# Kernel optimization log

Hardware: AMD Instinct MI355X
Metric: run time of the kernel (lower is better)

The kernel has to match this reference:

```python
import jax, jax.numpy as jnp
import numpy as np

EPS = 1e-8
MIN_VAL = -1e7  # min_val for masked_max padding


def _cos(v1, v2, axis=-1):
    # torch.F.cosine_similarity: dot / (max(||v1||,eps) * max(||v2||,eps))
    n1 = jnp.maximum(jnp.linalg.norm(v1, axis=axis), EPS)
    n2 = jnp.maximum(jnp.linalg.norm(v2, axis=axis), EPS)
    return jnp.sum(v1 * v2, axis=axis) / (n1 * n2)


def _mpm(v1, v2, w):
    # v1: (B,S,H), v2: (B,S,H) or (B,1,H), w: (P,H)
    mv_one = _cos(v1, v2)[..., None]                 # (B,S,1)
    v1w = w[None, None] * v1[:, :, None, :]          # (B,S,P,H)
    v2w = w[None, None] * v2[:, :, None, :]          # (B,S or 1,P,H)
    mv_many = _cos(v1w, v2w)                          # (B,S,P)
    return mv_one, mv_many


def _mpm_pairwise(v1, v2, w):
    # v1: (B,S1,H), v2: (B,S2,H), w: (P,H) -> (B,S1,S2,P)
    v1w = w[None, :, None, :] * v1[:, None]          # (B,P,S1,H)
    v2w = w[None, :, None, :] * v2[:, None]          # (B,P,S2,H)
    n1 = jnp.linalg.norm(v1w, axis=3)[..., None]     # (B,P,S1,1)
    n2 = jnp.linalg.norm(v2w, axis=3)[..., None]     # (B,P,S2,1)
    mul = jnp.einsum('bpih,bpjh->bpij', v1w, v2w)    # (B,P,S1,S2)
    norm = jnp.maximum(n1 * jnp.swapaxes(n2, 2, 3), EPS)
    return jnp.transpose(mul / norm, (0, 2, 3, 1))


def _masked_max(v, m, axis, keepdims=False):
    return jnp.max(v + (1.0 - m) * MIN_VAL, axis=axis, keepdims=keepdims)


def _masked_mean(v, m, axis, keepdims=False):
    s = jnp.sum(v, axis=axis, keepdims=keepdims)
    c = jnp.sum(m, axis=axis, keepdims=keepdims)
    return s / jnp.maximum(c, EPS)


def _bimpm(context_p, mask_p, context_h, mask_h, w_full, w_maxpool, w_att, w_maxatt):
    mp = mask_p.astype(context_p.dtype)              # (B,S1)
    mh = mask_h.astype(context_h.dtype)              # (B,S2)
    len_p = jnp.sum(mask_p, axis=1)
    len_h = jnp.sum(mask_h, axis=1)
    cp = context_p * mp[..., None]
    ch = context_h * mh[..., None]

    # pairwise cosine similarity (B,S1,S2)
    cos = _cos(cp[:, :, None, :], ch[:, None, :, :])
    cos_max_p = _masked_max(cos, mh[:, None, :], 2, True)
    cos_mean_p = _masked_mean(cos, mh[:, None, :], 2, True)
    cosT = jnp.swapaxes(cos, 1, 2)
    cos_max_h = _masked_max(cosT, mp[:, None, :], 2, True)
    cos_mean_h = _masked_mean(cosT, mp[:, None, :], 2, True)
    mv_p = [cos_max_p, cos_mean_p]
    mv_h = [cos_max_h, cos_mean_h]

    # full match (is_forward=True -> use last valid token)
    B, _, H = cp.shape
    idx_p = jnp.maximum(len_p - 1, 0)[:, None, None]
    idx_h = jnp.maximum(len_h - 1, 0)[:, None, None]
    last_p = jnp.take_along_axis(cp, jnp.broadcast_to(idx_p, (B, 1, H)), axis=1)
    last_h = jnp.take_along_axis(ch, jnp.broadcast_to(idx_h, (B, 1, H)), axis=1)
    o, m = _mpm(cp, last_h, w_full); mv_p += [o, m]
    o, m = _mpm(ch, last_p, w_full); mv_h += [o, m]

    # maxpool match over pairwise multi-perspective cosines (B,S1,S2,P)
    pw = _mpm_pairwise(cp, ch, w_maxpool)
    mv_p += [_masked_max(pw, mh[:, None, :, None], 2),
             _masked_mean(pw, mh[:, None, :, None], 2)]
    pwT = jnp.transpose(pw, (0, 2, 1, 3))
    mv_h += [_masked_max(pwT, mp[:, None, :, None], 2),
             _masked_mean(pwT, mp[:, None, :, None], 2)]

    # attentive match (mean-weighted by cosine attention)
    att = cos
    att_mean_h = jnp.einsum('bij,bjh->bih', att, ch) / jnp.maximum(
        jnp.sum(att, axis=2, keepdims=True), EPS)        # (B,S1,H)
    att_mean_p = jnp.einsum('bij,bih->bjh', att, cp) / jnp.maximum(
        jnp.swapaxes(jnp.sum(att, axis=1, keepdims=True), 1, 2), EPS)  # (B,S2,H)
    o, m = _mpm(cp, att_mean_h, w_att); mv_p += [o, m]
    o, m = _mpm(ch, att_mean_p, w_att); mv_h += [o, m]

    # max attentive match
    att_h_full = ch[:, None, :, :] * att[..., None]      # (B,S1,S2,H)
    att_max_h = _masked_max(att_h_full, mh[:, None, :, None], 2)  # (B,S1,H)
    att_p_full = cp[:, :, None, :] * att[..., None]      # (B,S1,S2,H)
    att_max_p = _masked_max(att_p_full, mp[:, :, None, None], 1)  # (B,S2,H)
    o, m = _mpm(cp, att_max_h, w_maxatt); mv_p += [o, m]
    o, m = _mpm(ch, att_max_p, w_maxatt); mv_h += [o, m]

    # (2, B, S, output_dim=105)
    return jnp.stack([jnp.concatenate(mv_p, axis=-1),
                      jnp.concatenate(mv_h, axis=-1)], axis=0)


def setup_inputs() -> dict:
    B, S1, S2, H, P = 8, 256, 256, 100, 20
    key = jax.random.key(0)
    ks = jax.random.split(key, 8)
    context_p = jax.random.normal(ks[0], (B, S1, H), jnp.float32)
    context_h = jax.random.normal(ks[1], (B, S2, H), jnp.float32)
    len_p = jax.random.randint(ks[2], (B,), S1 // 2, S1 + 1)
    len_h = jax.random.randint(ks[3], (B,), S2 // 2, S2 + 1)
    mask_p = (jnp.arange(S1)[None, :] < len_p[:, None]).astype(jnp.int32)
    mask_h = (jnp.arange(S2)[None, :] < len_h[:, None]).astype(jnp.int32)
    # four matching weights (share_weight_between_directions=True), torch.rand -> U[0,1)
    w_full = jax.random.uniform(ks[4], (P, H), jnp.float32)
    w_maxpool = jax.random.uniform(ks[5], (P, H), jnp.float32)
    w_att = jax.random.uniform(ks[6], (P, H), jnp.float32)
    w_maxatt = jax.random.uniform(ks[7], (P, H), jnp.float32)
    return {"context_p": context_p, "mask_p": mask_p, "context_h": context_h,
            "mask_h": mask_h, "w_full": w_full, "w_maxpool": w_maxpool,
            "w_att": w_att, "w_maxatt": w_maxatt}


def reference(context_p, mask_p, context_h, mask_h, w_full, w_maxpool, w_att, w_maxatt):
    return _bimpm(context_p, mask_p, context_h, mask_h, w_full, w_maxpool, w_att, w_maxatt)
```

## Files before the change

kernel.cpp:

```cpp
#include <hip/hip_runtime.h>

#define Bq 8
#define Sq 256
#define Hq 100
#define Pq 20
#define PPq 21
#define Fq 105
#define EPSq 1e-8f
#define NEGB -1e30f
#define IMG (128 * 136)

typedef short bf16x8 __attribute__((ext_vector_type(8)));
typedef float f32x4 __attribute__((ext_vector_type(4)));

__device__ __forceinline__ unsigned fkey(float f) {
    unsigned b = __float_as_uint(f);
    return (b & 0x80000000u) ? ~b : (b | 0x80000000u);
}
__device__ __forceinline__ float funkey(unsigned k) {
    return __uint_as_float((k & 0x80000000u) ? (k ^ 0x80000000u) : ~k);
}
__device__ __forceinline__ unsigned short bf16rn(float f) {
    unsigned u = __float_as_uint(f);
    unsigned r = u + 0x7FFFu + ((u >> 16) & 1u);
    return (unsigned short)(r >> 16);
}
__device__ __forceinline__ unsigned mulpack(unsigned pair, float w0, float w1) {
    float f0 = __uint_as_float(pair << 16);
    float f1 = __uint_as_float(pair & 0xFFFF0000u);
    f0 *= w0; f1 *= w1;
    return ((unsigned)bf16rn(f0)) | (((unsigned)bf16rn(f1)) << 16);
}

__global__ __launch_bounds__(256) void k_prep(
    const float* __restrict__ ctx_p, const int* __restrict__ mask_p,
    const float* __restrict__ ctx_h, const int* __restrict__ mask_h,
    const float* __restrict__ w_mp,
    float* __restrict__ vm, float* __restrict__ vmT,
    float* __restrict__ mf, float* __restrict__ wn,
    unsigned short* __restrict__ a16,
    float* __restrict__ lens, int* __restrict__ lasts,
    unsigned* __restrict__ statinit) {
    __shared__ float tileT[Hq * 65];
    __shared__ float w2T[Hq * 20];
    __shared__ float redp[PPq * 4 * 64];
    __shared__ float smf[64];
    __shared__ int ired[256];
    int blk = blockIdx.x;
    int side = blk >> 5;
    int b = (blk >> 2) & 7;
    int sq = blk & 3;
    int s0 = sq * 64;
    int t = threadIdx.x;

    for (int idx = blk * 256 + t; idx < 4 * Bq * PPq * Sq; idx += 64 * 256)
        statinit[idx] = 0u;

    const float* ctx = side ? ctx_h : ctx_p;
    const int* mask = side ? mask_h : mask_p;
    ired[t] = mask[b * Sq + t];
    if (t < 64) smf[t] = (float)mask[b * Sq + s0 + t];
    for (int idx = t; idx < Pq * Hq; idx += 256) {
        int p = idx / Hq, h = idx - p * Hq;
        float w = w_mp[idx];
        w2T[h * 20 + p] = w * w;
    }
    __syncthreads();
    if (sq == 0) {
        for (int o = 128; o; o >>= 1) {
            if (t < o) ired[t] += ired[t + o];
            __syncthreads();
        }
        if (t == 0) {
            int l = ired[0];
            lens[side * Bq + b] = (float)l;
            lasts[side * Bq + b] = l > 0 ? l - 1 : 0;
        }
    }

    unsigned short* abase = a16 + (size_t)(side * Bq + b) * 2 * IMG;
    {
        ushort4 z = {0, 0, 0, 0};
        for (int idx = t; idx < 576; idx += 256) {
            int r = idx / 9, c = idx - r * 9;
            int g = s0 + r;
            *(ushort4*)(abase + (g >> 7) * IMG + (g & 127) * 136 + 100 + c * 4) = z;
        }
    }

    const float4* src = (const float4*)(ctx + ((size_t)b * Sq + s0) * Hq);
    float4* vmo = (float4*)(vm + ((size_t)side * Bq + b) * Sq * Hq + (size_t)s0 * Hq);
#pragma unroll
    for (int q = 0; q < 7; q++) {
        int F = t + 256 * q;
        if (F < 1600) {
            int s = F / 25, c = F - s * 25;
            float m = smf[s];
            float4 v4 = src[F];
            v4.x *= m; v4.y *= m; v4.z *= m; v4.w *= m;
            vmo[F] = v4;
            int h0 = c * 4;
            tileT[(h0 + 0) * 65 + s] = v4.x;
            tileT[(h0 + 1) * 65 + s] = v4.y;
            tileT[(h0 + 2) * 65 + s] = v4.z;
            tileT[(h0 + 3) * 65 + s] = v4.w;
            int g = s0 + s;
            ushort4 o;
            o.x = bf16rn(v4.x); o.y = bf16rn(v4.y); o.z = bf16rn(v4.z); o.w = bf16rn(v4.w);
            *(ushort4*)(abase + (g >> 7) * IMG + (g & 127) * 136 + c * 4) = o;
        }
    }
    __syncthreads();

    int sl = t & 63, hq = t >> 6;
    float acc[PPq];
#pragma unroll
    for (int p = 0; p < PPq; p++) acc[p] = 0.f;
    float* vmTo = vmT + ((size_t)side * Bq + b) * Hq * Sq + s0;
    int hbeg = hq * 25;
#pragma unroll 5
    for (int h = hbeg; h < hbeg + 25; h++) {
        float v = tileT[h * 65 + sl];
        vmTo[(size_t)h * Sq + sl] = v;
        float e = v * v;
        acc[Pq] += e;
        const float4* wrow = (const float4*)(w2T + h * 20);
#pragma unroll
        for (int pq = 0; pq < 5; pq++) {
            float4 w4 = wrow[pq];
            acc[pq * 4 + 0] += w4.x * e;
            acc[pq * 4 + 1] += w4.y * e;
            acc[pq * 4 + 2] += w4.z * e;
            acc[pq * 4 + 3] += w4.w * e;
        }
    }
#pragma unroll
    for (int p = 0; p < PPq; p++)
        redp[(p * 4 + hq) * 64 + sl] = acc[p];
    __syncthreads();

    float* wout = wn + ((size_t)side * Bq + b) * PPq * Sq + s0;
    for (int idx = t; idx < PPq * 64; idx += 256) {
        int p = idx >> 6, s2 = idx & 63;
        float ssum = redp[(p * 4 + 0) * 64 + s2] + redp[(p * 4 + 1) * 64 + s2] +
                     redp[(p * 4 + 2) * 64 + s2] + redp[(p * 4 + 3) * 64 + s2];
        wout[p * Sq + s2] = 1.f / fmaxf(sqrtf(ssum), EPSq);
    }
    if (t < 64) mf[(size_t)side * Bq * Sq + b * Sq + s0 + t] = smf[t];
}

__global__ __launch_bounds__(256) void k_pw(
    const unsigned short* __restrict__ a16,
    const float* __restrict__ vmT,
    const float* __restrict__ wn, const float* __restrict__ mf,
    const float* __restrict__ w_mp, const float* __restrict__ lens,
    float* __restrict__ out, float* __restrict__ cosm, float* __restrict__ cosT,
    unsigned* __restrict__ rowmax, float* __restrict__ rowsum,
    unsigned* __restrict__ colmax, float* __restrict__ colsum) {
    __shared__ unsigned short As[128 * 72];
    __shared__ unsigned short Bs[128 * 72];
    __shared__ float w2s[144];
    int blk = blockIdx.x;
    int t = threadIdx.x;

    if (blk >= 64) {
        int mblk = blk - 64;
        int b = mblk / 80;
        int rem = mblk - b * 80;
        int p = rem >> 2;
        int ih = (rem >> 1) & 1, jh = rem & 1;
        int i0 = ih * 128, j0 = jh * 128;

        if (t < 144) {
            float w = (t < Hq) ? w_mp[p * Hq + t] : 0.f;
            w2s[t] = w * w;
        }
        __syncthreads();

        const uint4* sa = (const uint4*)(a16 + (size_t)(b * 2 + ih) * IMG);
        const uint4* sb = (const uint4*)(a16 + (size_t)((Bq + b) * 2 + jh) * IMG);
        uint4* dA = (uint4*)As;
        uint4* dB = (uint4*)Bs;

        int lane = t & 63;
        int wv = t >> 6;
        int wr = wv & 1, wc = wv >> 1;
        int lm = lane & 15, lq = lane >> 4;

        f32x4 acc[4][4];
#pragma unroll
        for (int tm = 0; tm < 4; tm++)
#pragma unroll
            for (int tn = 0; tn < 4; tn++) acc[tm][tn] = 0.f;

#pragma unroll
        for (int q = 0; q < 2; q++) {
#pragma unroll
            for (int it = 0; it < 4; it++) {
                int idx = t + 256 * it;
                int row = idx >> 3, cc = idx & 7;
                dA[row * 9 + cc] = sa[row * 17 + q * 8 + cc];
                int hb = (q * 8 + cc) * 8;
                uint4 ch = sb[row * 17 + q * 8 + cc];
                float4 wA = *(const float4*)(w2s + hb);
                float4 wB = *(const float4*)(w2s + hb + 4);
                uint4 o;
                o.x = mulpack(ch.x, wA.x, wA.y);
                o.y = mulpack(ch.y, wA.z, wA.w);
                o.z = mulpack(ch.z, wB.x, wB.y);
                o.w = mulpack(ch.w, wB.z, wB.w);
                dB[row * 9 + cc] = o;
            }
            __syncthreads();
#pragma unroll
            for (int ksl = 0; ksl < 2; ksl++) {
                bf16x8 af[4], bfr[4];
#pragma unroll
                for (int tm = 0; tm < 4; tm++)
                    af[tm] = *(const bf16x8*)&As[(wr * 64 + tm * 16 + lm) * 72 + ksl * 32 + lq * 8];
#pragma unroll
                for (int tn = 0; tn < 4; tn++)
                    bfr[tn] = *(const bf16x8*)&Bs[(wc * 64 + tn * 16 + lm) * 72 + ksl * 32 + lq * 8];
#pragma unroll
                for (int tm = 0; tm < 4; tm++)
#pragma unroll
                    for (int tn = 0; tn < 4; tn++)
                        acc[tm][tn] = __builtin_amdgcn_mfma_f32_16x16x32_bf16(af[tm], bfr[tn], acc[tm][tn], 0, 0, 0);
            }
            __syncthreads();
        }

        const float* wn0 = wn + ((size_t)b * PPq + p) * Sq;
        const float* wn1 = wn + ((size_t)(Bq + b) * PPq + p) * Sq;
        const float* mfp = mf + b * Sq;
        const float* mfh = mf + (size_t)Bq * Sq + b * Sq;
        size_t base = ((size_t)b * PPq + p) * Sq;
        float rn2v[4], mzh[4];
#pragma unroll
        for (int tn = 0; tn < 4; tn++) {
            int jj = j0 + wc * 64 + tn * 16 + lm;
            rn2v[tn] = wn1[jj];
            mzh[tn] = mfh[jj] > 0.5f ? 0.f : NEGB;
        }
        float cmax[4] = {NEGB, NEGB, NEGB, NEGB};
        float csum[4] = {0.f, 0.f, 0.f, 0.f};
#pragma unroll
        for (int tm = 0; tm < 4; tm++) {
            int ibase = i0 + wr * 64 + tm * 16 + lq * 4;
            float rn1v[4], mzp[4];
#pragma unroll
            for (int r2 = 0; r2 < 4; r2++) {
                rn1v[r2] = wn0[ibase + r2];
                mzp[r2] = mfp[ibase + r2] > 0.5f ? 0.f : NEGB;
            }
            float rmax[4] = {NEGB, NEGB, NEGB, NEGB};
            float rsum[4] = {0.f, 0.f, 0.f, 0.f};
#pragma unroll
            for (int tn = 0; tn < 4; tn++)
#pragma unroll
                for (int r2 = 0; r2 < 4; r2++) {
                    float v = acc[tm][tn][r2] * rn1v[r2] * rn2v[tn];
                    rmax[r2] = fmaxf(rmax[r2], v + mzh[tn]);
                    rsum[r2] += v;
                    cmax[tn] = fmaxf(cmax[tn], v + mzp[r2]);
                    csum[tn] += v;
                }
#pragma unroll
            for (int r2 = 0; r2 < 4; r2++)
#pragma unroll
                for (int o = 1; o < 16; o <<= 1) {
                    rmax[r2] = fmaxf(rmax[r2], __shfl_xor(rmax[r2], o, 64));
                    rsum[r2] += __shfl_xor(rsum[r2], o, 64);
                }
            if (lm == 0) {
#pragma unroll
                for (int r2 = 0; r2 < 4; r2++) {
                    atomicMax(rowmax + base + ibase + r2, fkey(rmax[r2]));
                    atomicAdd(rowsum + base + ibase + r2, rsum[r2]);
                }
            }
        }
#pragma unroll
        for (int tn = 0; tn < 4; tn++) {
#pragma unroll
            for (int o = 16; o < 64; o <<= 1) {
                cmax[tn] = fmaxf(cmax[tn], __shfl_xor(cmax[tn], o, 64));
                csum[tn] += __shfl_xor(csum[tn], o, 64);
            }
        }
        if (lq == 0) {
#pragma unroll
            for (int tn = 0; tn < 4; tn++) {
                int jj = j0 + wc * 64 + tn * 16 + lm;
                atomicMax(colmax + base + jj, fkey(cmax[tn]));
                atomicAdd(colsum + base + jj, csum[tn]);
            }
        }
        return;
    }

    float (*cbmax)[Sq] = (float (*)[Sq])As;
    float (*cbsum)[Sq] = (float (*)[Sq])(As + 4096);
    int b = blk >> 3, it = blk & 7;
    int lane = t & 63;
    int wid = __builtin_amdgcn_readfirstlane(t >> 6);
    int i0 = it * 32 + wid * 8;

    const float* abase2 = vmT + (size_t)b * Hq * Sq;
    const float* bbase2 = vmT + (size_t)(Bq + b) * Hq * Sq;

    float4 acc[8];
#pragma unroll
    for (int k = 0; k < 8; k++) acc[k] = make_float4(0.f, 0.f, 0.f, 0.f);

#pragma unroll 4
    for (int h = 0; h < Hq; h++) {
        float4 bq = ((const float4*)(bbase2 + h * Sq))[lane];
        const float4* ap = (const float4*)(abase2 + h * Sq + i0);
        float4 a0 = ap[0], a1 = ap[1];
        float av[8] = {a0.x, a0.y, a0.z, a0.w, a1.x, a1.y, a1.z, a1.w};
#pragma unroll
        for (int k = 0; k < 8; k++) {
            acc[k].x += av[k] * bq.x; acc[k].y += av[k] * bq.y;
            acc[k].z += av[k] * bq.z; acc[k].w += av[k] * bq.w;
        }
    }

    const float* wn0 = wn + ((size_t)b * PPq + Pq) * Sq;
    const float* wn1 = wn + ((size_t)(Bq + b) * PPq + Pq) * Sq;
    float4 rn2 = ((const float4*)wn1)[lane];
    float4 mh4 = ((const float4*)(mf + (size_t)Bq * Sq + b * Sq))[lane];
    float invLh = 1.f / fmaxf(lens[Bq + b], EPSq);

    float cmax[4] = {NEGB, NEGB, NEGB, NEGB};
    float csum[4] = {0.f, 0.f, 0.f, 0.f};
#pragma unroll
    for (int k = 0; k < 8; k++) {
        float r1 = wn0[i0 + k];
        float4 v;
        v.x = acc[k].x * r1 * rn2.x;
        v.y = acc[k].y * r1 * rn2.y;
        v.z = acc[k].z * r1 * rn2.z;
        v.w = acc[k].w * r1 * rn2.w;
        float m0 = mh4.x > 0.5f ? v.x : NEGB;
        float m1 = mh4.y > 0.5f ? v.y : NEGB;
        float m2 = mh4.z > 0.5f ? v.z : NEGB;
        float m3 = mh4.w > 0.5f ? v.w : NEGB;
        float rmax = fmaxf(fmaxf(m0, m1), fmaxf(m2, m3));
        float rs = v.x + v.y + v.z + v.w;
        for (int o = 32; o; o >>= 1) {
            rmax = fmaxf(rmax, __shfl_xor(rmax, o, 64));
            rs += __shfl_xor(rs, o, 64);
        }
        if (lane == 0) {
            float* orow = out + ((size_t)(b * Sq + i0 + k)) * Fq;
            orow[0] = rmax;
            orow[1] = rs * invLh;
        }
        float mi = mf[b * Sq + i0 + k];
        if (mi > 0.5f) {
            cmax[0] = fmaxf(cmax[0], v.x); cmax[1] = fmaxf(cmax[1], v.y);
            cmax[2] = fmaxf(cmax[2], v.z); cmax[3] = fmaxf(cmax[3], v.w);
        }
        csum[0] += v.x; csum[1] += v.y; csum[2] += v.z; csum[3] += v.w;
        ((float4*)(cosm + (size_t)(b * Sq + i0 + k) * Sq))[lane] = v;
        int jb = 4 * lane;
        cosT[((size_t)b * Sq + jb + 0) * Sq + i0 + k] = v.x;
        cosT[((size_t)b * Sq + jb + 1) * Sq + i0 + k] = v.y;
        cosT[((size_t)b * Sq + jb + 2) * Sq + i0 + k] = v.z;
        cosT[((size_t)b * Sq + jb + 3) * Sq + i0 + k] = v.w;
    }
    ((float4*)&cbmax[wid][0])[lane] = make_float4(cmax[0], cmax[1], cmax[2], cmax[3]);
    ((float4*)&cbsum[wid][0])[lane] = make_float4(csum[0], csum[1], csum[2], csum[3]);
    __syncthreads();
    {
        int j = t;
        float mx = fmaxf(fmaxf(cbmax[0][j], cbmax[1][j]), fmaxf(cbmax[2][j], cbmax[3][j]));
        float sm = cbsum[0][j] + cbsum[1][j] + cbsum[2][j] + cbsum[3][j];
        size_t cidx = ((size_t)b * PPq + Pq) * Sq + j;
        atomicMax(colmax + cidx, fkey(mx));
        atomicAdd(colsum + cidx, sm);
    }
}

__global__ __launch_bounds__(256) void k_att(
    const float* __restrict__ vm, const float* __restrict__ mf,
    const float* __restrict__ cosm, const float* __restrict__ cosT,
    const unsigned* __restrict__ rowmax, const float* __restrict__ rowsum,
    const unsigned* __restrict__ colmax, const float* __restrict__ colsum,
    const float* __restrict__ lens,
    float* __restrict__ out,
    float* __restrict__ attvT) {
    __shared__ float L[Sq * 8];
    __shared__ float bm[Sq];
    __shared__ float pam[2][8][128];
    __shared__ float pax[2][8][128];
    int blk = blockIdx.x;
    int t = threadIdx.x;
    int d = blk >> 8;
    int rem = blk & 255;
    int b = rem >> 5, rt = rem & 31;
    int r0 = rt * 8;

    if (blk < Bq * PPq) {
        int bcf = blk / PPq, pcf = blk - bcf * PPq;
        float mx = funkey(colmax[(size_t)blk * Sq + t]);
        float sm = colsum[(size_t)blk * Sq + t];
        float invLp = 1.f / fmaxf(lens[bcf], EPSq);
        float* orow = out + (size_t)Bq * Sq * Fq + (size_t)(bcf * Sq + t) * Fq;
        if (pcf < Pq) { orow[23 + pcf] = mx; orow[43 + pcf] = sm * invLp; }
        else { orow[0] = mx; orow[1] = sm * invLp; }
    } else if (blk < 2 * Bq * PPq) {
        int rf = blk - Bq * PPq;
        int bcf = rf / PPq, pcf = rf - bcf * PPq;
        if (pcf < Pq) {
            float mx = funkey(rowmax[(size_t)(bcf * PPq + pcf) * Sq + t]);
            float sm = rowsum[(size_t)(bcf * PPq + pcf) * Sq + t];
            float invLh = 1.f / fmaxf(lens[Bq + bcf], EPSq);
            float* orow = out + (size_t)(bcf * Sq + t) * Fq;
            orow[23 + pcf] = mx; orow[43 + pcf] = sm * invLh;
        }
    }
    bm[t] = (mf[(size_t)(1 - d) * Bq * Sq + b * Sq + t] > 0.5f) ? 0.f : NEGB;

    const float* src = (d ? cosm : cosT) + (size_t)b * Sq * Sq;
#pragma unroll
    for (int q = 0; q < 2; q++) {
        int F = t + 256 * q;
        int k = F >> 1, c = F & 1;
        float4 v4 = *(const float4*)(src + (size_t)k * Sq + r0 + c * 4);
        *(float4*)(L + k * 8 + c * 4) = v4;
    }
    __syncthreads();

    int h = t & 127, kh = t >> 7;
    const float* vB = vm + (size_t)(1 - d) * Bq * Sq * Hq + (size_t)b * Sq * Hq + h;
    bool hv = (h < Hq);
    float am[8], ax[8];
#pragma unroll
    for (int r = 0; r < 8; r++) { am[r] = 0.f; ax[r] = NEGB; }
    int k0 = kh * 128;
#pragma unroll 16
    for (int kk = 0; kk < 128; kk++) {
        int k = k0 + kk;
        float v = hv ? vB[(size_t)k * Hq] : 0.f;
        float4 w0 = *(const float4*)(L + k * 8);
        float4 w1 = *(const float4*)(L + k * 8 + 4);
        float bk = bm[k];
        float wv[8] = {w0.x, w0.y, w0.z, w0.w, w1.x, w1.y, w1.z, w1.w};
#pragma unroll
        for (int r = 0; r < 8; r++) {
            float pr = wv[r] * v;
            am[r] += pr;
            ax[r] = fmaxf(ax[r], pr + bk);
        }
    }
#pragma unroll
    for (int r = 0; r < 8; r++) { pam[kh][r][h] = am[r]; pax[kh][r][h] = ax[r]; }
    __syncthreads();
    if (t < Hq) {
        float4 m0, m1, x0, x1;
        m0.x = pam[0][0][t] + pam[1][0][t]; x0.x = fmaxf(pax[0][0][t], pax[1][0][t]);
        m0.y = pam[0][1][t] + pam[1][1][t]; x0.y = fmaxf(pax[0][1][t], pax[1][1][t]);
        m0.z = pam[0][2][t] + pam[1][2][t]; x0.z = fmaxf(pax[0][2][t], pax[1][2][t]);
        m0.w = pam[0][3][t] + pam[1][3][t]; x0.w = fmaxf(pax[0][3][t], pax[1][3][t]);
        m1.x = pam[0][4][t] + pam[1][4][t]; x1.x = fmaxf(pax[0][4][t], pax[1][4][t]);
        m1.y = pam[0][5][t] + pam[1][5][t]; x1.y = fmaxf(pax[0][5][t], pax[1][5][t]);
        m1.z = pam[0][6][t] + pam[1][6][t]; x1.z = fmaxf(pax[0][6][t], pax[1][6][t]);
        m1.w = pam[0][7][t] + pam[1][7][t]; x1.w = fmaxf(pax[0][7][t], pax[1][7][t]);
        float* om = attvT + (((size_t)(d * 2 + 0) * Bq + b) * Hq + t) * Sq + r0;
        float* ox = attvT + (((size_t)(d * 2 + 1) * Bq + b) * Hq + t) * Sq + r0;
        *(float4*)om = m0; *(float4*)(om + 4) = m1;
        *(float4*)ox = x0; *(float4*)(ox + 4) = x1;
    }
}

__global__ __launch_bounds__(128) void k_final(
    const float* __restrict__ vm, const float* __restrict__ vmT,
    const int* __restrict__ lasts, const float* __restrict__ attvT,
    const float* __restrict__ w_full, const float* __restrict__ w_att,
    const float* __restrict__ w_maxatt,
    float* __restrict__ out) {
    __shared__ float w2s[Hq * 2];
    __shared__ float v2u[Hq];
    int blk = blockIdx.x;
    int m = blk / 320;
    int rem = blk - m * 320;
    int dir = rem / 160; rem -= dir * 160;
    int b = rem / 20;    rem -= b * 20;
    int sc = rem / 10;
    int ps = rem - sc * 10;
    int t = threadIdx.x;
    const float* W = (m == 0) ? w_full : (m == 1) ? w_att : w_maxatt;
    for (int idx = t; idx < 2 * Hq; idx += 128) {
        int pp = idx / Hq, h = idx - pp * Hq;
        float w = W[(ps * 2 + pp) * Hq + h];
        w2s[h * 2 + pp] = w * w;
    }
    if (m == 0 && t < Hq) {
        int lastO = dir ? lasts[b] : lasts[Bq + b];
        v2u[t] = vm[(size_t)(1 - dir) * Bq * Sq * Hq + ((size_t)b * Sq + lastO) * Hq + t];
    }
    __syncthreads();

    int s = sc * 128 + t;
    const float* v1T = vmT + (size_t)(dir * Bq + b) * Hq * Sq + s;
    const float* v2T = attvT + ((size_t)(dir * 2 + (m == 2 ? 1 : 0)) * Bq + b) * Hq * Sq + s;

    float d0 = 0.f, a0 = 0.f, b0 = 0.f;
    float d1 = 0.f, a1 = 0.f, b1 = 0.f;
    float pd = 0.f, p1 = 0.f, p2 = 0.f;
#pragma unroll 4
    for (int h = 0; h < Hq; h++) {
        float v1 = v1T[h * Sq];
        float v2 = (m == 0) ? v2u[h] : v2T[h * Sq];
        float e1 = v1 * v2, e2 = v1 * v1, e3 = v2 * v2;
        float w0 = w2s[h * 2], w1 = w2s[h * 2 + 1];
        d0 += w0 * e1; a0 += w0 * e2; b0 += w0 * e3;
        d1 += w1 * e1; a1 += w1 * e2; b1 += w1 * e3;
        if (ps == 0) { pd += e1; p1 += e2; p2 += e3; }
    }
    int fbase = (m == 0) ? 2 : (m == 1) ? 63 : 84;
    float* orow = out + (size_t)dir * Bq * Sq * Fq + ((size_t)b * Sq + s) * Fq;
    if (ps == 0)
        orow[fbase] = pd / (fmaxf(sqrtf(p1), EPSq) * fmaxf(sqrtf(p2), EPSq));
    orow[fbase + 1 + ps * 2]     = d0 / (fmaxf(sqrtf(a0), EPSq) * fmaxf(sqrtf(b0), EPSq));
    orow[fbase + 1 + ps * 2 + 1] = d1 / (fmaxf(sqrtf(a1), EPSq) * fmaxf(sqrtf(b1), EPSq));
}

extern "C" void kernel_launch(void* const* d_in, const int* in_sizes, int n_in,
                              void* d_out, int out_size, void* d_ws, size_t ws_size,
                              hipStream_t stream) {
    (void)in_sizes; (void)n_in; (void)out_size; (void)ws_size;
    const float* ctx_p    = (const float*)d_in[0];
    const int*   mask_p   = (const int*)d_in[1];
    const float* ctx_h    = (const float*)d_in[2];
    const int*   mask_h   = (const int*)d_in[3];
    const float* w_full   = (const float*)d_in[4];
    const float* w_maxpool= (const float*)d_in[5];
    const float* w_att    = (const float*)d_in[6];
    const float* w_maxatt = (const float*)d_in[7];
    float* out = (float*)d_out;
    float* ws = (float*)d_ws;

    const size_t BSH = (size_t)Bq * Sq * Hq;
    const size_t BS  = (size_t)Bq * Sq;
    const size_t BSS = (size_t)Bq * Sq * Sq;
    const size_t BPS = (size_t)Bq * PPq * Sq;

    float* vm     = ws;               ws += 2 * BSH;
    float* vmT    = ws;               ws += 2 * BSH;
    unsigned short* a16 = (unsigned short*)ws;  ws += 2 * Bq * IMG / 2 * 2;
    float* mf     = ws;               ws += 2 * BS;
    float* wn     = ws;               ws += 2 * BPS;
    float* cosm   = ws;               ws += BSS;
    float* cosT   = ws;               ws += BSS;
    unsigned* rowmax = (unsigned*)ws; ws += BPS;
    float* rowsum = ws;               ws += BPS;
    unsigned* colmax = (unsigned*)ws; ws += BPS;
    float* colsum = ws;               ws += BPS;
    float* attvT  = ws;               ws += 4 * BSH;
    float* lens   = ws;               ws += 16;
    int*   lasts  = (int*)ws;         ws += 16;

    k_prep<<<64, 256, 0, stream>>>(ctx_p, mask_p, ctx_h, mask_h, w_maxpool,
                                   vm, vmT, mf, wn, a16, lens, lasts, rowmax);
    k_pw<<<704, 256, 0, stream>>>(a16, vmT, wn, mf, w_maxpool, lens,
                                  out, cosm, cosT, rowmax, rowsum, colmax, colsum);
    k_att<<<512, 256, 0, stream>>>(vm, mf, cosm, cosT, rowmax, rowsum, colmax, colsum,
                                   lens, out, attvT);
    k_final<<<960, 128, 0, stream>>>(vm, vmT, lasts, attvT, w_full, w_att, w_maxatt, out);
}
```

Measured before the change: 135.2 us.

## Fuse attentive-matching cosine kernel into attention kernel, dropping attvT round trip

The final multi-perspective cosine computation (full, attentive and max-attentive matching) moves into the attention kernel. It works on the eight attention rows already held in shared memory, with squared weights and the v1 rows staged in LDS. This removes one kernel launch and the global write and read of the attvT intermediate. In exchange, each of the 512 blocks now recomputes the squared weight table, uses much more shared memory (about 25 KB of extra LDS), and runs a serial 100-step dot loop over 504 tasks, which may reduce occupancy.

```diff
diff --git a/kernel.cpp b/kernel.cpp
--- a/kernel.cpp
+++ b/kernel.cpp
@@ -383,18 +383,24 @@
     }
 }
 
-__global__ __launch_bounds__(256) void k_att(
+__global__ __launch_bounds__(256) void k_attf(
     const float* __restrict__ vm, const float* __restrict__ mf,
     const float* __restrict__ cosm, const float* __restrict__ cosT,
     const unsigned* __restrict__ rowmax, const float* __restrict__ rowsum,
     const unsigned* __restrict__ colmax, const float* __restrict__ colsum,
-    const float* __restrict__ lens,
-    float* __restrict__ out,
-    float* __restrict__ attvT) {
+    const float* __restrict__ lens, const int* __restrict__ lasts,
+    const float* __restrict__ w_full, const float* __restrict__ w_att,
+    const float* __restrict__ w_maxatt,
+    float* __restrict__ out) {
     __shared__ float L[Sq * 8];
     __shared__ float bm[Sq];
     __shared__ float pam[2][8][128];
     __shared__ float pax[2][8][128];
+    __shared__ float Lw2[3 * Hq * 21];
+    __shared__ float Lv1[8 * 104];
+    __shared__ float Lam[8 * 104];
+    __shared__ float Lax[8 * 104];
+    __shared__ float Lv2u[104];
     int blk = blockIdx.x;
     int t = threadIdx.x;
     int d = blk >> 8;
@@ -423,6 +429,28 @@
     }
     bm[t] = (mf[(size_t)(1 - d) * Bq * Sq + b * Sq + t] > 0.5f) ? 0.f : NEGB;
 
+    for (int idx = t; idx < 3 * Pq * Hq; idx += 256) {
+        int m = idx / (Pq * Hq);
+        int rem2 = idx - m * (Pq * Hq);
+        int p = rem2 / Hq, h = rem2 - p * Hq;
+        const float* W = (m == 0) ? w_full : (m == 1) ? w_att : w_maxatt;
+        float w = W[p * Hq + h];
+        Lw2[(m * Hq + h) * 21 + p] = w * w;
+    }
+    for (int idx = t; idx < 3 * Hq; idx += 256) {
+        int m = idx / Hq, h = idx - m * Hq;
+        Lw2[(m * Hq + h) * 21 + 20] = 1.f;
+    }
+    for (int idx = t; idx < 8 * Hq; idx += 256) {
+        int r = idx / Hq, h = idx - r * Hq;
+        Lv1[r * 104 + h] =
+            vm[(size_t)d * Bq * Sq * Hq + ((size_t)b * Sq + r0 + r) * Hq + h];
+    }
+    if (t < Hq) {
+        int lastO = d ? lasts[b] : lasts[Bq + b];
+        Lv2u[t] = vm[(size_t)(1 - d) * Bq * Sq * Hq + ((size_t)b * Sq + lastO) * Hq + t];
+    }
+
     const float* src = (d ? cosm : cosT) + (size_t)b * Sq * Sq;
 #pragma unroll
     for (int q = 0; q < 2; q++) {
@@ -459,73 +487,33 @@
     for (int r = 0; r < 8; r++) { pam[kh][r][h] = am[r]; pax[kh][r][h] = ax[r]; }
     __syncthreads();
     if (t < Hq) {
-        float4 m0, m1, x0, x1;
-        m0.x = pam[0][0][t] + pam[1][0][t]; x0.x = fmaxf(pax[0][0][t], pax[1][0][t]);
-        m0.y = pam[0][1][t] + pam[1][1][t]; x0.y = fmaxf(pax[0][1][t], pax[1][1][t]);
-        m0.z = pam[0][2][t] + pam[1][2][t]; x0.z = fmaxf(pax[0][2][t], pax[1][2][t]);
-        m0.w = pam[0][3][t] + pam[1][3][t]; x0.w = fmaxf(pax[0][3][t], pax[1][3][t]);
-        m1.x = pam[0][4][t] + pam[1][4][t]; x1.x = fmaxf(pax[0][4][t], pax[1][4][t]);
-        m1.y = pam[0][5][t] + pam[1][5][t]; x1.y = fmaxf(pax[0][5][t], pax[1][5][t]);
-        m1.z = pam[0][6][t] + pam[1][6][t]; x1.z = fmaxf(pax[0][6][t], pax[1][6][t]);
-        m1.w = pam[0][7][t] + pam[1][7][t]; x1.w = fmaxf(pax[0][7][t], pax[1][7][t]);
-        float* om = attvT + (((size_t)(d * 2 + 0) * Bq + b) * Hq + t) * Sq + r0;
-        float* ox = attvT + (((size_t)(d * 2 + 1) * Bq + b) * Hq + t) * Sq + r0;
-        *(float4*)om = m0; *(float4*)(om + 4) = m1;
-        *(float4*)ox = x0; *(float4*)(ox + 4) = x1;
-    }
-}
-
-__global__ __launch_bounds__(128) void k_final(
-    const float* __restrict__ vm, const float* __restrict__ vmT,
-    const int* __restrict__ lasts, const float* __restrict__ attvT,
-    const float* __restrict__ w_full, const float* __restrict__ w_att,
-    const float* __restrict__ w_maxatt,
-    float* __restrict__ out) {
-    __shared__ float w2s[Hq * 2];
-    __shared__ float v2u[Hq];
-    int blk = blockIdx.x;
-    int m = blk / 320;
-    int rem = blk - m * 320;
-    int dir = rem / 160; rem -= dir * 160;
-    int b = rem / 20;    rem -= b * 20;
-    int sc = rem / 10;
-    int ps = rem - sc * 10;
-    int t = threadIdx.x;
-    const float* W = (m == 0) ? w_full : (m == 1) ? w_att : w_maxatt;
-    for (int idx = t; idx < 2 * Hq; idx += 128) {
-        int pp = idx / Hq, h = idx - pp * Hq;
-        float w = W[(ps * 2 + pp) * Hq + h];
-        w2s[h * 2 + pp] = w * w;
-    }
-    if (m == 0 && t < Hq) {
-        int lastO = dir ? lasts[b] : lasts[Bq + b];
-        v2u[t] = vm[(size_t)(1 - dir) * Bq * Sq * Hq + ((size_t)b * Sq + lastO) * Hq + t];
-    }
-    __syncthreads();
-
-    int s = sc * 128 + t;
-    const float* v1T = vmT + (size_t)(dir * Bq + b) * Hq * Sq + s;
-    const float* v2T = attvT + ((size_t)(dir * 2 + (m == 2 ? 1 : 0)) * Bq + b) * Hq * Sq + s;
-
-    float d0 = 0.f, a0 = 0.f, b0 = 0.f;
-    float d1 = 0.f, a1 = 0.f, b1 = 0.f;
-    float pd = 0.f, p1 = 0.f, p2 = 0.f;
+#pragma unroll
+        for (int r = 0; r < 8; r++) {
+            Lam[r * 104 + t] = pam[0][r][t] + pam[1][r][t];
+            Lax[r * 104 + t] = fmaxf(pax[0][r][t], pax[1][r][t]);
+        }
+    }
+    __syncthreads();
+
+    size_t orow_base = (size_t)d * Bq * Sq * Fq + ((size_t)b * Sq + r0) * Fq;
+    for (int task = t; task < 504; task += 256) {
+        int r = task & 7;
+        int mp = task >> 3;
+        int m = mp / 21, p = mp - m * 21;
+        const float* v1p = Lv1 + r * 104;
+        const float* v2p = (m == 0) ? Lv2u : (m == 1 ? Lam + r * 104 : Lax + r * 104);
+        const float* wp = Lw2 + m * Hq * 21 + p;
+        float dd = 0.f, aa = 0.f, bb = 0.f;
 #pragma unroll 4
-    for (int h = 0; h < Hq; h++) {
-        float v1 = v1T[h * Sq];
-        float v2 = (m == 0) ? v2u[h] : v2T[h * Sq];
-        float e1 = v1 * v2, e2 = v1 * v1, e3 = v2 * v2;
-        float w0 = w2s[h * 2], w1 = w2s[h * 2 + 1];
-        d0 += w0 * e1; a0 += w0 * e2; b0 += w0 * e3;
-        d1 += w1 * e1; a1 += w1 * e2; b1 += w1 * e3;
-        if (ps == 0) { pd += e1; p1 += e2; p2 += e3; }
-    }
-    int fbase = (m == 0) ? 2 : (m == 1) ? 63 : 84;
-    float* orow = out + (size_t)dir * Bq * Sq * Fq + ((size_t)b * Sq + s) * Fq;
-    if (ps == 0)
-        orow[fbase] = pd / (fmaxf(sqrtf(p1), EPSq) * fmaxf(sqrtf(p2), EPSq));
-    orow[fbase + 1 + ps * 2]     = d0 / (fmaxf(sqrtf(a0), EPSq) * fmaxf(sqrtf(b0), EPSq));
-    orow[fbase + 1 + ps * 2 + 1] = d1 / (fmaxf(sqrtf(a1), EPSq) * fmaxf(sqrtf(b1), EPSq));
+        for (int hh = 0; hh < Hq; hh++) {
+            float v1 = v1p[hh], v2 = v2p[hh], w = wp[hh * 21];
+            dd += w * v1 * v2; aa += w * v1 * v1; bb += w * v2 * v2;
+        }
+        int fbase = (m == 0) ? 2 : (m == 1) ? 63 : 84;
+        int col = (p < 20) ? (fbase + 1 + p) : fbase;
+        out[orow_base + (size_t)r * Fq + col] =
+            dd / (fmaxf(sqrtf(aa), EPSq) * fmaxf(sqrtf(bb), EPSq));
+    }
 }
 
 extern "C" void kernel_launch(void* const* d_in, const int* in_sizes, int n_in,
@@ -559,7 +547,6 @@
     float* rowsum = ws;               ws += BPS;
     unsigned* colmax = (unsigned*)ws; ws += BPS;
     float* colsum = ws;               ws += BPS;
-    float* attvT  = ws;               ws += 4 * BSH;
     float* lens   = ws;               ws += 16;
     int*   lasts  = (int*)ws;         ws += 16;
 
@@ -567,7 +554,6 @@
                                    vm, vmT, mf, wn, a16, lens, lasts, rowmax);
     k_pw<<<704, 256, 0, stream>>>(a16, vmT, wn, mf, w_maxpool, lens,
                                   out, cosm, cosT, rowmax, rowsum, colmax, colsum);
-    k_att<<<512, 256, 0, stream>>>(vm, mf, cosm, cosT, rowmax, rowsum, colmax, colsum,
-                                   lens, out, attvT);
-    k_final<<<960, 128, 0, stream>>>(vm, vmT, lasts, attvT, w_full, w_att, w_maxatt, out);
-}
+    k_attf<<<512, 256, 0, stream>>>(vm, mf, cosm, cosT, rowmax, rowsum, colmax, colsum,
+                                    lens, lasts, w_full, w_att, w_maxatt, out);
+}
```

New measurement: 129.6 us. -4.2%, faster.
